# Kernel tuning notes

Measured on AMD Instinct MI355X. Metric: run time of the kernel, lower is better.

## Reference

```python
import jax, jax.numpy as jnp
import numpy as np

D_MODEL = 1024
NHEAD = 16
HEAD_DIM = D_MODEL // NHEAD
MAX_LEN = 4096
ROPE_BASE = 500.0


def _rope_tables(L, dim):
    inv_freq = 1.0 / (ROPE_BASE ** (jnp.arange(0, dim, 2, dtype=jnp.float32) / dim))
    t = jnp.arange(L, dtype=jnp.float32)
    freqs = jnp.einsum('i,j->ij', t, inv_freq)  # [L, dim/2]
    emb = jnp.concatenate([freqs, freqs], axis=-1)  # [L, dim]
    return jnp.cos(emb), jnp.sin(emb)


def _rotate_half(x):
    x1, x2 = jnp.split(x, 2, axis=-1)
    return jnp.concatenate([-x2, x1], axis=-1)


def _apply_rope(x, cos, sin):
    return x * cos + _rotate_half(x) * sin


def setup_inputs() -> dict:
    key = jax.random.key(0)
    ks = jax.random.split(key, 6)
    B, L = 4, 2048
    bound_qkv = 1.0 / np.sqrt(D_MODEL)
    x = jax.random.normal(ks[0], (B, L, D_MODEL), dtype=jnp.float32)
    key_padding_mask = jnp.zeros((B, L), dtype=bool)
    W_qkv = jax.random.uniform(ks[1], (3 * D_MODEL, D_MODEL), jnp.float32, -bound_qkv, bound_qkv)
    b_qkv = jax.random.uniform(ks[2], (3 * D_MODEL,), jnp.float32, -bound_qkv, bound_qkv)
    W_out = jax.random.uniform(ks[3], (D_MODEL, D_MODEL), jnp.float32, -bound_qkv, bound_qkv)
    b_out = jax.random.uniform(ks[4], (D_MODEL,), jnp.float32, -bound_qkv, bound_qkv)
    return {"x": x, "key_padding_mask": key_padding_mask,
            "W_qkv": W_qkv, "b_qkv": b_qkv, "W_out": W_out, "b_out": b_out}


def reference(x, key_padding_mask, W_qkv, b_qkv, W_out, b_out):
    B, L, D = x.shape
    H, hd = NHEAD, HEAD_DIM
    qkv = x @ W_qkv.T + b_qkv  # [B, L, 3D]
    q, k, v = jnp.split(qkv, 3, axis=-1)
    # [B, H, L, hd]
    q = q.reshape(B, L, H, hd).transpose(0, 2, 1, 3)
    k = k.reshape(B, L, H, hd).transpose(0, 2, 1, 3)
    v = v.reshape(B, L, H, hd).transpose(0, 2, 1, 3)
    cos, sin = _rope_tables(L, hd)  # [L, hd]
    q = _apply_rope(q, cos, sin)
    k = _apply_rope(k, cos, sin)
    scores = jnp.einsum('bhqd,bhkd->bhqk', q, k) / jnp.sqrt(jnp.float32(hd))
    mask = key_padding_mask[:, None, None, :]  # [B,1,1,L]
    scores = jnp.where(mask, -jnp.inf, scores)
    attn = jax.nn.softmax(scores, axis=-1)
    out = jnp.einsum('bhqk,bhkd->bhqd', attn, v)
    out = out.transpose(0, 2, 1, 3).reshape(B, L, D)
    return out @ W_out.T + b_out
```

## Files before the change

kernel.cpp:

```cpp
#include <hip/hip_runtime.h>
#include <stdint.h>

typedef __attribute__((ext_vector_type(8))) __bf16 bf16x8;
typedef __attribute__((ext_vector_type(4))) short short4v;
typedef __attribute__((ext_vector_type(4))) float f32x4;

#if __has_builtin(__builtin_amdgcn_exp2f)
#define EXP2(x) __builtin_amdgcn_exp2f(x)
#else
#define EXP2(x) exp2f(x)
#endif

__device__ __forceinline__ short f2bf(float f) {
  union { float f; uint32_t u; } v; v.f = f;
  uint32_t r = (v.u + 0x7fffu + ((v.u >> 16) & 1u)) >> 16;
  return (short)(uint16_t)r;
}

__device__ __forceinline__ uint32_t pk2bf(float a, float b) {
  union { __bf16 h; uint16_t u; } x, y;
  x.h = (__bf16)a; y.h = (__bf16)b;
  return (uint32_t)x.u | ((uint32_t)y.u << 16);
}

__device__ __forceinline__ void gl2lds16(const void* g, const void* lds) {
  __builtin_amdgcn_global_load_lds(
      (const __attribute__((address_space(1))) void*)(uintptr_t)g,
      (__attribute__((address_space(3))) void*)(uint32_t)(uintptr_t)lds,
      16, 0, 0);
}

__device__ __forceinline__ bf16x8 frag8(const short* p) {
  return *(const bf16x8*)(const void*)p;
}

__global__ void convert3_k(const float* __restrict__ s0, short* __restrict__ d0, int n0,
                           const float* __restrict__ s1, short* __restrict__ d1, int n1,
                           const float* __restrict__ s2, short* __restrict__ d2, int n2) {
  int i = blockIdx.x * blockDim.x + threadIdx.x;
  int t0 = n0 >> 2, t1 = t0 + (n1 >> 2), t2 = t1 + (n2 >> 2);
  const float* s; short* d; int off;
  if (i < t0) { s = s0; d = d0; off = i; }
  else if (i < t1) { s = s1; d = d1; off = i - t0; }
  else if (i < t2) { s = s2; d = d2; off = i - t1; }
  else return;
  float4 v = ((const float4*)s)[off];
  short4v o;
  o.x = f2bf(v.x); o.y = f2bf(v.y); o.z = f2bf(v.z); o.w = f2bf(v.w);
  *(short4v*)(d + off * 4) = o;
}

__global__ void rope_tab_k(float* __restrict__ cosT, float* __restrict__ sinT,
                           const unsigned char* __restrict__ mask, float* __restrict__ maskf) {
  int i = blockIdx.x * blockDim.x + threadIdx.x;
  int j = i >> 11, pos = i & 2047;
  float invf = exp2f(-(float)j * (8.965784284662087f / 32.0f));
  float ang = (float)pos * invf;
  float s, c;
  sincosf(ang, &s, &c);
  cosT[i] = c; sinT[i] = s;
  if (i < 8192) maskf[i] = mask[i] ? -1e30f : 0.0f;
}

template <int EPI>
__global__ __launch_bounds__(256, 3)
void gemm_bt_k(const short* __restrict__ A, const short* __restrict__ Bm,
               const float* __restrict__ bias, int N, int K,
               float* __restrict__ Cout,
               const float* __restrict__ cosT, const float* __restrict__ sinT,
               short* __restrict__ Qb, short* __restrict__ Kb, short* __restrict__ Vt) {
  __shared__ short As[3][128 * 32];
  __shared__ short Bs[3][128 * 32];
  const int tid = threadIdx.x;
  const int lane = tid & 63;
  const int w = tid >> 6;
  const int g = lane >> 4, l15 = lane & 15;
  const int wm = (w >> 1) * 64, wn = (w & 1) * 64;
  const int bm = (EPI == 1) ? blockIdx.y : blockIdx.x;
  const int bn = (EPI == 1) ? blockIdx.x : blockIdx.y;

  const int rseg = lane >> 2;
  const int cofs = ((lane & 3) ^ ((lane >> 3) & 3)) * 8;
  const int sA0 = w, sA1 = w + 4;
  const int arow0 = (bm * 128 + sA0 * 16 + rseg) * K;
  const int arow1 = (bm * 128 + sA1 * 16 + rseg) * K;
  const int brow0 = (bn * 128 + sA0 * 16 + rseg) * K;
  const int brow1 = (bn * 128 + sA1 * 16 + rseg) * K;

  const int rsw = (l15 >> 1) & 3;

  f32x4 acc[4][4];
#pragma unroll
  for (int i = 0; i < 4; i++)
#pragma unroll
    for (int j = 0; j < 4; j++) acc[i][j] = f32x4{0.f, 0.f, 0.f, 0.f};

#pragma unroll
  for (int t = 0; t < 2; t++) {
    gl2lds16(A + arow0 + t * 32 + cofs, &As[t][sA0 * 512]);
    gl2lds16(A + arow1 + t * 32 + cofs, &As[t][sA1 * 512]);
    gl2lds16(Bm + brow0 + t * 32 + cofs, &Bs[t][sA0 * 512]);
    gl2lds16(Bm + brow1 + t * 32 + cofs, &Bs[t][sA1 * 512]);
  }

  const int K32 = K >> 5;
  int cur = 0, pre = 2;
  for (int kt = 0; kt < K32; kt++) {
    if (kt < K32 - 1) { asm volatile("s_waitcnt vmcnt(4)" ::: "memory"); }
    else              { asm volatile("s_waitcnt vmcnt(0)" ::: "memory"); }
    __builtin_amdgcn_s_barrier();

    if (kt + 2 < K32) {
      const int k2 = (kt + 2) * 32;
      gl2lds16(A + arow0 + k2 + cofs, &As[pre][sA0 * 512]);
      gl2lds16(A + arow1 + k2 + cofs, &As[pre][sA1 * 512]);
      gl2lds16(Bm + brow0 + k2 + cofs, &Bs[pre][sA0 * 512]);
      gl2lds16(Bm + brow1 + k2 + cofs, &Bs[pre][sA1 * 512]);
    }
    bf16x8 af[4], bf[4];
#pragma unroll
    for (int im = 0; im < 4; im++) af[im] = frag8(&As[cur][(wm + im * 16 + l15) * 32 + (g ^ rsw) * 8]);
#pragma unroll
    for (int jn = 0; jn < 4; jn++) bf[jn] = frag8(&Bs[cur][(wn + jn * 16 + l15) * 32 + (g ^ rsw) * 8]);
#pragma unroll
    for (int im = 0; im < 4; im++)
#pragma unroll
      for (int jn = 0; jn < 4; jn++)
        acc[im][jn] = __builtin_amdgcn_mfma_f32_16x16x32_bf16(af[im], bf[jn], acc[im][jn], 0, 0, 0);

    cur = (cur == 2) ? 0 : cur + 1;
    pre = (pre == 2) ? 0 : pre + 1;
  }

  const int row0 = bm * 128 + wm + g * 4;
  const int col0 = bn * 128 + wn;

  if (EPI == 0) {
#pragma unroll
    for (int jn = 0; jn < 4; jn++) {
      float bb = bias[col0 + jn * 16 + l15];
#pragma unroll
      for (int im = 0; im < 4; im++)
#pragma unroll
        for (int r = 0; r < 4; r++) {
          int row = row0 + im * 16 + r;
          Cout[row * N + col0 + jn * 16 + l15] = acc[im][jn][r] + bb;
        }
    }
  } else {
#pragma unroll
    for (int jn = 0; jn < 4; jn++) {
      float bb = bias[col0 + jn * 16 + l15];
#pragma unroll
      for (int im = 0; im < 4; im++)
#pragma unroll
        for (int r = 0; r < 4; r++) acc[im][jn][r] += bb;
    }
    const int sector = col0 >> 10;
    const int h = (col0 & 1023) >> 6;
    if (sector == 2) {
#pragma unroll
      for (int jn = 0; jn < 4; jn++) {
        int d = jn * 16 + l15;
#pragma unroll
        for (int im = 0; im < 4; im++) {
          int row = row0 + im * 16;
          int b = row >> 11, pos = row & 2047;
          union { uint32_t u[2]; short4v s4; } pw;
          pw.u[0] = pk2bf(acc[im][jn][0], acc[im][jn][1]);
          pw.u[1] = pk2bf(acc[im][jn][2], acc[im][jn][3]);
          *(short4v*)&Vt[((b * 16 + h) * 64 + d) * 2048 + pos] = pw.s4;
        }
      }
    } else {
      short* dst = (sector == 0) ? Qb : Kb;
      const float scl = (sector == 0) ? 0.18033688011112042f : 1.0f;
      const int posb = row0 & 2047;
      const int bq = row0 >> 11;
#pragma unroll
      for (int jn = 0; jn < 4; jn++) {
        int d = jn * 16 + l15;
        int j = d & 31;
        const float* cp = cosT + j * 2048;
        const float* sp = sinT + j * 2048;
#pragma unroll
        for (int im = 0; im < 4; im++) {
          f32x4 cv = *(const f32x4*)(cp + posb + im * 16);
          f32x4 sn = *(const f32x4*)(sp + posb + im * 16);
#pragma unroll
          for (int r = 0; r < 4; r++) {
            int pos = posb + im * 16 + r;
            float xv = acc[im][jn][r];
            float xp = acc[im][jn ^ 2][r];
            float rot = (jn < 2) ? -xp : xp;
            dst[((bq * 16 + h) * 2048 + pos) * 64 + d] = f2bf((xv * cv[r] + rot * sn[r]) * scl);
          }
        }
      }
    }
  }
}

__global__ __launch_bounds__(256, 4)
void attn_k(const short* __restrict__ Qb, const short* __restrict__ Kb,
            const short* __restrict__ Vt, const float* __restrict__ maskf,
            short* __restrict__ attn) {
  __shared__ short Ks[3][32 * 64];
  __shared__ short Vs[3][64 * 32];
  __shared__ short Ps[4][32 * 32];
  __shared__ float Ms[2048];
  const int tid = threadIdx.x, lane = tid & 63, w = tid >> 6;
  const int g = lane >> 4, l15 = lane & 15;
  const int swk = l15 & 7;
  const int fv = (l15 ^ (l15 >> 2)) & 3;
  const int swz = (blockIdx.x & 7) * 128 + (blockIdx.x >> 3);
  const int qt = swz & 15, bh = swz >> 4;
  const int b = bh >> 4, h = bh & 15;

  bf16x8 aq[2][2];
#pragma unroll
  for (int qi = 0; qi < 2; qi++)
#pragma unroll
    for (int kc = 0; kc < 2; kc++) {
      int q = qt * 128 + w * 32 + qi * 16 + l15;
      aq[qi][kc] = *(const bf16x8*)(const void*)(Qb + (bh * 2048 + q) * 64 + kc * 32 + g * 8);
    }
  bf16x8 aone;
#pragma unroll
  for (int i = 0; i < 8; i++) aone[i] = (__bf16)1.0f;

  f32x4 o[4][2];
#pragma unroll
  for (int jd = 0; jd < 4; jd++)
#pragma unroll
    for (int qi = 0; qi < 2; qi++) o[jd][qi] = f32x4{0.f, 0.f, 0.f, 0.f};
  f32x4 lacc[2] = {f32x4{0.f, 0.f, 0.f, 0.f}, f32x4{0.f, 0.f, 0.f, 0.f}};

  bf16x8 av[4], bp[2];
#pragma unroll
  for (int jd = 0; jd < 4; jd++)
#pragma unroll
    for (int i = 0; i < 8; i++) av[jd][i] = (__bf16)0.0f;
#pragma unroll
  for (int qi = 0; qi < 2; qi++)
#pragma unroll
    for (int i = 0; i < 8; i++) bp[qi][i] = (__bf16)0.0f;

  const float* mfp = maskf + b * 2048;

  const int kr8 = lane >> 3;
  const int kcst = (lane & 7) ^ kr8;
  const int vrs = lane >> 2;
  const int vcs = (lane & 3) ^ ((vrs ^ (vrs >> 2)) & 3);

#pragma unroll
  for (int i = 0; i < 2; i++) {
    int s = w * 2 + i;
    gl2lds16(mfp + s * 256 + lane * 4, &Ms[s * 256]);
  }
  if (w < 2) {
#pragma unroll
    for (int t = 0; t < 2; t++)
#pragma unroll
      for (int i = 0; i < 2; i++) {
        int s = (w & 1) * 2 + i;
        gl2lds16(Kb + (bh * 2048 + t * 32 + s * 8 + kr8) * 64 + kcst * 8, &Ks[t][s * 512]);
      }
  } else {
#pragma unroll
    for (int t = 0; t < 2; t++)
#pragma unroll
      for (int i = 0; i < 2; i++) {
        int s = (w & 1) * 2 + i;
        gl2lds16(Vt + (bh * 64 + s * 16 + vrs) * 2048 + t * 32 + vcs * 8, &Vs[t][s * 512]);
      }
  }

  int cur = 0, pre = 2;
  for (int kt = 0; kt < 64; kt++) {
    if (kt < 62) {
      asm volatile("s_waitcnt vmcnt(2)" ::: "memory");
    } else {
      asm volatile("s_waitcnt vmcnt(0)" ::: "memory");
    }
    __builtin_amdgcn_s_barrier();

    if (kt < 62) {
      const int nb = (kt + 2) * 32;
      if (w < 2) {
#pragma unroll
        for (int i = 0; i < 2; i++) {
          int s = (w & 1) * 2 + i;
          gl2lds16(Kb + (bh * 2048 + nb + s * 8 + kr8) * 64 + kcst * 8, &Ks[pre][s * 512]);
        }
      } else {
#pragma unroll
        for (int i = 0; i < 2; i++) {
          int s = (w & 1) * 2 + i;
          gl2lds16(Vt + (bh * 64 + s * 16 + vrs) * 2048 + nb + vcs * 8, &Vs[pre][s * 512]);
        }
      }
    }

    __builtin_amdgcn_s_setprio(1);
#pragma unroll
    for (int qi = 0; qi < 2; qi++) {
#pragma unroll
      for (int jd = 0; jd < 4; jd++)
        o[jd][qi] = __builtin_amdgcn_mfma_f32_16x16x32_bf16(av[jd], bp[qi], o[jd][qi], 0, 0, 0);
      lacc[qi] = __builtin_amdgcn_mfma_f32_16x16x32_bf16(aone, bp[qi], lacc[qi], 0, 0, 0);
    }
    __builtin_amdgcn_s_setprio(0);

    const int kbase = kt * 32;
    f32x4 sv[2][2];
#pragma unroll
    for (int kvt = 0; kvt < 2; kvt++) {
      f32x4 mf = *(const f32x4*)(const void*)&Ms[kbase + kvt * 16 + g * 4];
      sv[kvt][0] = mf; sv[kvt][1] = mf;
    }
    __builtin_amdgcn_s_setprio(1);
#pragma unroll
    for (int kvt = 0; kvt < 2; kvt++)
#pragma unroll
      for (int kc = 0; kc < 2; kc++) {
        bf16x8 ak = frag8(&Ks[cur][(kvt * 16 + l15) * 64 + ((kc * 4 + g) ^ swk) * 8]);
        sv[kvt][0] = __builtin_amdgcn_mfma_f32_16x16x32_bf16(ak, aq[0][kc], sv[kvt][0], 0, 0, 0);
        sv[kvt][1] = __builtin_amdgcn_mfma_f32_16x16x32_bf16(ak, aq[1][kc], sv[kvt][1], 0, 0, 0);
      }
    __builtin_amdgcn_s_setprio(0);

#pragma unroll
    for (int jd = 0; jd < 4; jd++)
      av[jd] = frag8(&Vs[cur][(jd * 16 + l15) * 32 + (g ^ fv) * 8]);

#pragma unroll
    for (int qi = 0; qi < 2; qi++)
#pragma unroll
      for (int kvt = 0; kvt < 2; kvt++) {
        union { uint32_t u[2]; short4v s4; } pw;
        pw.u[0] = pk2bf(EXP2(sv[kvt][qi][0]), EXP2(sv[kvt][qi][1]));
        pw.u[1] = pk2bf(EXP2(sv[kvt][qi][2]), EXP2(sv[kvt][qi][3]));
        *(short4v*)&Ps[w][(qi * 16 + l15) * 32 + (((kvt * 2 + (g >> 1)) ^ fv) * 8) + (g & 1) * 4] = pw.s4;
      }
#pragma unroll
    for (int qi = 0; qi < 2; qi++)
      bp[qi] = frag8(&Ps[w][(qi * 16 + l15) * 32 + (g ^ fv) * 8]);

    cur = (cur == 2) ? 0 : cur + 1;
    pre = (pre == 2) ? 0 : pre + 1;
  }

  __builtin_amdgcn_s_setprio(1);
#pragma unroll
  for (int qi = 0; qi < 2; qi++) {
#pragma unroll
    for (int jd = 0; jd < 4; jd++)
      o[jd][qi] = __builtin_amdgcn_mfma_f32_16x16x32_bf16(av[jd], bp[qi], o[jd][qi], 0, 0, 0);
    lacc[qi] = __builtin_amdgcn_mfma_f32_16x16x32_bf16(aone, bp[qi], lacc[qi], 0, 0, 0);
  }
  __builtin_amdgcn_s_setprio(0);

#pragma unroll
  for (int qi = 0; qi < 2; qi++) {
    float inv = 1.0f / lacc[qi][0];
    int q = qt * 128 + w * 32 + qi * 16 + l15;
#pragma unroll
    for (int jd = 0; jd < 4; jd++) {
      union { uint32_t u[2]; short4v s4; } pw;
      pw.u[0] = pk2bf(o[jd][qi][0] * inv, o[jd][qi][1] * inv);
      pw.u[1] = pk2bf(o[jd][qi][2] * inv, o[jd][qi][3] * inv);
      *(short4v*)&attn[(b * 2048 + q) * 1024 + h * 64 + jd * 16 + g * 4] = pw.s4;
    }
  }
}

extern "C" void kernel_launch(void* const* d_in, const int* in_sizes, int n_in,
                              void* d_out, int out_size, void* d_ws, size_t ws_size,
                              hipStream_t stream) {
  const float* x = (const float*)d_in[0];
  const unsigned char* mask = (const unsigned char*)d_in[1];
  const float* W_qkv = (const float*)d_in[2];
  const float* b_qkv = (const float*)d_in[3];
  const float* W_out = (const float*)d_in[4];
  const float* b_out = (const float*)d_in[5];
  float* out = (float*)d_out;

  char* ws = (char*)d_ws;
  short* xb    = (short*)(ws + 0);
  short* wqkvb = (short*)(ws + 16777216);
  short* woutb = (short*)(ws + 23068672);
  float* cosT  = (float*)(ws + 25165824);
  float* sinT  = (float*)(ws + 25427968);
  short* Qb    = (short*)(ws + 25690112);
  short* Kb    = (short*)(ws + 42467328);
  short* Vtb   = (short*)(ws + 59244544);
  short* attnb = (short*)(ws + 76021760);
  float* maskf = (float*)(ws + 92798976);

  convert3_k<<<12288, 256, 0, stream>>>(x, xb, 8388608, W_qkv, wqkvb, 3145728, W_out, woutb, 1048576);
  rope_tab_k<<<256, 256, 0, stream>>>(cosT, sinT, mask, maskf);
  gemm_bt_k<1><<<dim3(24, 64), 256, 0, stream>>>(xb, wqkvb, b_qkv, 3072, 1024,
                                                 nullptr, cosT, sinT, Qb, Kb, Vtb);
  attn_k<<<dim3(1024), 256, 0, stream>>>(Qb, Kb, Vtb, maskf, attnb);
  gemm_bt_k<0><<<dim3(64, 8), 256, 0, stream>>>(attnb, woutb, b_out, 1024, 1024,
                                                out, nullptr, nullptr, nullptr, nullptr, nullptr);
}
```

Baseline: 286.9 us.

## Use 256x256-tile 512-thread GEMM with direct-to-LDS loads for QKV projection

The QKV projection now runs on a new kernel with 256x256 output tiles, 8 waves, K-step 64 and double-buffered LDS filled through global-to-LDS loads. It also uses a swizzled block order and raises wave priority around the MFMA bursts. The larger tile raises arithmetic intensity and cuts global traffic per FLOP, at the cost of 128KB of LDS and much higher register pressure. The output projection keeps the old kernel with its RoPE/QKV epilogue removed.

```diff
diff --git a/kernel.cpp b/kernel.cpp
--- a/kernel.cpp
+++ b/kernel.cpp
@@ -63,12 +63,169 @@
 }
 
 template <int EPI>
-__global__ __launch_bounds__(256, 3)
-void gemm_bt_k(const short* __restrict__ A, const short* __restrict__ Bm,
+__global__ __launch_bounds__(512, 2)
+void gemm256_k(const short* __restrict__ A, const short* __restrict__ Bm,
                const float* __restrict__ bias, int N, int K,
                float* __restrict__ Cout,
                const float* __restrict__ cosT, const float* __restrict__ sinT,
                short* __restrict__ Qb, short* __restrict__ Kb, short* __restrict__ Vt) {
+  __shared__ short As[2][256 * 64];
+  __shared__ short Bs[2][256 * 64];
+  const int tid = threadIdx.x;
+  const int lane = tid & 63;
+  const int w = tid >> 6;
+  const int wr = w >> 2, wc = w & 3;
+  const int g = lane >> 4, l15 = lane & 15;
+
+  int bm, bn;
+  if (EPI == 1) {
+    const int swz = (blockIdx.x & 7) * 48 + (blockIdx.x >> 3);
+    bm = swz / 12; bn = swz % 12;
+  } else {
+    bm = blockIdx.x; bn = blockIdx.y;
+  }
+  const int rowA0 = bm * 256;
+  const int rowB0 = bn * 256;
+
+  const int rl = tid >> 3;
+  const int cl = tid & 7;
+  const int sc8 = (cl ^ (rl & 7)) * 8;
+  const int ldso = w * 512;
+  const int swz7 = l15 & 7;
+
+  f32x4 acc[8][4];
+#pragma unroll
+  for (int i = 0; i < 8; i++)
+#pragma unroll
+    for (int j = 0; j < 4; j++) acc[i][j] = f32x4{0.f, 0.f, 0.f, 0.f};
+
+  auto stageT = [&](int kt) {
+    short* dA = &As[kt & 1][0];
+    short* dB = &Bs[kt & 1][0];
+#pragma unroll
+    for (int hh = 0; hh < 2; ++hh)
+#pragma unroll
+      for (int s = 0; s < 2; ++s) {
+        const int r = hh * 128 + s * 64 + rl;
+        const int ld = (hh * 128 + s * 64) * 64 + ldso;
+        gl2lds16(A + (rowA0 + r) * K + kt * 64 + sc8, dA + ld);
+        gl2lds16(Bm + (rowB0 + r) * K + kt * 64 + sc8, dB + ld);
+      }
+  };
+
+  stageT(0);
+  asm volatile("s_waitcnt vmcnt(0)" ::: "memory");
+  __builtin_amdgcn_s_barrier();
+
+  for (int t = 0; t < 16; ++t) {
+    const short* as = &As[t & 1][0];
+    const short* bs = &Bs[t & 1][0];
+    bf16x8 bfr[4][2];
+#pragma unroll
+    for (int q = 0; q < 4; ++q) {
+      if (q == 0) {
+        if (t + 1 < 16) stageT(t + 1);
+#pragma unroll
+        for (int j = 0; j < 4; ++j)
+#pragma unroll
+          for (int kk = 0; kk < 2; ++kk)
+            bfr[j][kk] = frag8(&bs[(wc * 64 + j * 16 + l15) * 64 + (((kk * 4 + g) ^ swz7) * 8)]);
+      }
+      bf16x8 afr[2][2];
+#pragma unroll
+      for (int ii = 0; ii < 2; ++ii)
+#pragma unroll
+        for (int kk = 0; kk < 2; ++kk)
+          afr[ii][kk] = frag8(&as[(wr * 128 + (q * 2 + ii) * 16 + l15) * 64 + (((kk * 4 + g) ^ swz7) * 8)]);
+      __builtin_amdgcn_s_barrier();
+      __builtin_amdgcn_s_setprio(1);
+#pragma unroll
+      for (int ii = 0; ii < 2; ++ii)
+#pragma unroll
+        for (int j = 0; j < 4; ++j)
+#pragma unroll
+          for (int kk = 0; kk < 2; ++kk)
+            acc[q * 2 + ii][j] =
+                __builtin_amdgcn_mfma_f32_16x16x32_bf16(afr[ii][kk], bfr[j][kk], acc[q * 2 + ii][j], 0, 0, 0);
+      __builtin_amdgcn_s_setprio(0);
+      if (q == 3) asm volatile("s_waitcnt vmcnt(0)" ::: "memory");
+      __builtin_amdgcn_s_barrier();
+    }
+  }
+
+  const int row0 = rowA0 + wr * 128 + g * 4;
+  const int col0 = rowB0 + wc * 64;
+
+  if (EPI == 0) {
+#pragma unroll
+    for (int j = 0; j < 4; ++j) {
+      float bb = bias[col0 + j * 16 + l15];
+#pragma unroll
+      for (int i = 0; i < 8; ++i)
+#pragma unroll
+        for (int r = 0; r < 4; ++r) {
+          int row = row0 + i * 16 + r;
+          Cout[row * N + col0 + j * 16 + l15] = acc[i][j][r] + bb;
+        }
+    }
+  } else {
+#pragma unroll
+    for (int j = 0; j < 4; ++j) {
+      float bb = bias[col0 + j * 16 + l15];
+#pragma unroll
+      for (int i = 0; i < 8; ++i)
+#pragma unroll
+        for (int r = 0; r < 4; ++r) acc[i][j][r] += bb;
+    }
+    const int sector = col0 >> 10;
+    const int h = (col0 & 1023) >> 6;
+    const int posb = row0 & 2047;
+    const int bq = row0 >> 11;
+    if (sector == 2) {
+#pragma unroll
+      for (int j = 0; j < 4; ++j) {
+        int d = j * 16 + l15;
+#pragma unroll
+        for (int i = 0; i < 8; ++i) {
+          int pos = posb + i * 16;
+          union { uint32_t u[2]; short4v s4; } pw;
+          pw.u[0] = pk2bf(acc[i][j][0], acc[i][j][1]);
+          pw.u[1] = pk2bf(acc[i][j][2], acc[i][j][3]);
+          *(short4v*)&Vt[((bq * 16 + h) * 64 + d) * 2048 + pos] = pw.s4;
+        }
+      }
+    } else {
+      short* dst = (sector == 0) ? Qb : Kb;
+      const float scl = (sector == 0) ? 0.18033688011112042f : 1.0f;
+#pragma unroll
+      for (int j = 0; j < 4; ++j) {
+        int d = j * 16 + l15;
+        int jj = d & 31;
+        const float* cp = cosT + jj * 2048;
+        const float* sp = sinT + jj * 2048;
+#pragma unroll
+        for (int i = 0; i < 8; ++i) {
+          f32x4 cv = *(const f32x4*)(cp + posb + i * 16);
+          f32x4 sn = *(const f32x4*)(sp + posb + i * 16);
+#pragma unroll
+          for (int r = 0; r < 4; ++r) {
+            int pos = posb + i * 16 + r;
+            float xv = acc[i][j][r];
+            float xp = acc[i][j ^ 2][r];
+            float rot = (j < 2) ? -xp : xp;
+            dst[((bq * 16 + h) * 2048 + pos) * 64 + d] = f2bf((xv * cv[r] + rot * sn[r]) * scl);
+          }
+        }
+      }
+    }
+  }
+}
+
+template <int EPI>
+__global__ __launch_bounds__(256, 3)
+void gemm_bt_k(const short* __restrict__ A, const short* __restrict__ Bm,
+               const float* __restrict__ bias, int N, int K,
+               float* __restrict__ Cout) {
   __shared__ short As[3][128 * 32];
   __shared__ short Bs[3][128 * 32];
   const int tid = threadIdx.x;
@@ -76,8 +233,7 @@
   const int w = tid >> 6;
   const int g = lane >> 4, l15 = lane & 15;
   const int wm = (w >> 1) * 64, wn = (w & 1) * 64;
-  const int bm = (EPI == 1) ? blockIdx.y : blockIdx.x;
-  const int bn = (EPI == 1) ? blockIdx.x : blockIdx.y;
+  const int bm = blockIdx.x, bn = blockIdx.y;
 
   const int rseg = lane >> 2;
   const int cofs = ((lane & 3) ^ ((lane >> 3) & 3)) * 8;
@@ -134,70 +290,16 @@
 
   const int row0 = bm * 128 + wm + g * 4;
   const int col0 = bn * 128 + wn;
-
-  if (EPI == 0) {
-#pragma unroll
-    for (int jn = 0; jn < 4; jn++) {
-      float bb = bias[col0 + jn * 16 + l15];
-#pragma unroll
-      for (int im = 0; im < 4; im++)
-#pragma unroll
-        for (int r = 0; r < 4; r++) {
-          int row = row0 + im * 16 + r;
-          Cout[row * N + col0 + jn * 16 + l15] = acc[im][jn][r] + bb;
-        }
-    }
-  } else {
-#pragma unroll
-    for (int jn = 0; jn < 4; jn++) {
-      float bb = bias[col0 + jn * 16 + l15];
-#pragma unroll
-      for (int im = 0; im < 4; im++)
-#pragma unroll
-        for (int r = 0; r < 4; r++) acc[im][jn][r] += bb;
-    }
-    const int sector = col0 >> 10;
-    const int h = (col0 & 1023) >> 6;
-    if (sector == 2) {
-#pragma unroll
-      for (int jn = 0; jn < 4; jn++) {
-        int d = jn * 16 + l15;
-#pragma unroll
-        for (int im = 0; im < 4; im++) {
-          int row = row0 + im * 16;
-          int b = row >> 11, pos = row & 2047;
-          union { uint32_t u[2]; short4v s4; } pw;
-          pw.u[0] = pk2bf(acc[im][jn][0], acc[im][jn][1]);
-          pw.u[1] = pk2bf(acc[im][jn][2], acc[im][jn][3]);
-          *(short4v*)&Vt[((b * 16 + h) * 64 + d) * 2048 + pos] = pw.s4;
-        }
-      }
-    } else {
-      short* dst = (sector == 0) ? Qb : Kb;
-      const float scl = (sector == 0) ? 0.18033688011112042f : 1.0f;
-      const int posb = row0 & 2047;
-      const int bq = row0 >> 11;
-#pragma unroll
-      for (int jn = 0; jn < 4; jn++) {
-        int d = jn * 16 + l15;
-        int j = d & 31;
-        const float* cp = cosT + j * 2048;
-        const float* sp = sinT + j * 2048;
-#pragma unroll
-        for (int im = 0; im < 4; im++) {
-          f32x4 cv = *(const f32x4*)(cp + posb + im * 16);
-          f32x4 sn = *(const f32x4*)(sp + posb + im * 16);
-#pragma unroll
-          for (int r = 0; r < 4; r++) {
-            int pos = posb + im * 16 + r;
-            float xv = acc[im][jn][r];
-            float xp = acc[im][jn ^ 2][r];
-            float rot = (jn < 2) ? -xp : xp;
-            dst[((bq * 16 + h) * 2048 + pos) * 64 + d] = f2bf((xv * cv[r] + rot * sn[r]) * scl);
-          }
-        }
-      }
-    }
+#pragma unroll
+  for (int jn = 0; jn < 4; jn++) {
+    float bb = bias[col0 + jn * 16 + l15];
+#pragma unroll
+    for (int im = 0; im < 4; im++)
+#pragma unroll
+      for (int r = 0; r < 4; r++) {
+        int row = row0 + im * 16 + r;
+        Cout[row * N + col0 + jn * 16 + l15] = acc[im][jn][r] + bb;
+      }
   }
 }
 
@@ -400,9 +502,8 @@
 
   convert3_k<<<12288, 256, 0, stream>>>(x, xb, 8388608, W_qkv, wqkvb, 3145728, W_out, woutb, 1048576);
   rope_tab_k<<<256, 256, 0, stream>>>(cosT, sinT, mask, maskf);
-  gemm_bt_k<1><<<dim3(24, 64), 256, 0, stream>>>(xb, wqkvb, b_qkv, 3072, 1024,
-                                                 nullptr, cosT, sinT, Qb, Kb, Vtb);
+  gemm256_k<1><<<dim3(384), 512, 0, stream>>>(xb, wqkvb, b_qkv, 3072, 1024,
+                                              nullptr, cosT, sinT, Qb, Kb, Vtb);
   attn_k<<<dim3(1024), 256, 0, stream>>>(Qb, Kb, Vtb, maskf, attnb);
-  gemm_bt_k<0><<<dim3(64, 8), 256, 0, stream>>>(attnb, woutb, b_out, 1024, 1024,
-                                                out, nullptr, nullptr, nullptr, nullptr, nullptr);
-}
+  gemm_bt_k<0><<<dim3(64, 8), 256, 0, stream>>>(attnb, woutb, b_out, 1024, 1024, out);
+}
```

Measured after the change: 304.2 us. +6.0%, slower.
